# Performance work log

Measured on AMD Instinct MI355X. Metric: run time of the kernel, lower is better.

## Reference

```python
import jax, jax.numpy as jnp
import numpy as np

B, T, N, H = 512, 64, 512, 256  # batch, time steps, input_size, hidden_size
Tm1 = T - 1


def setup_inputs() -> dict:
    key = jax.random.key(0)
    ks = jax.random.split(key, 12)
    s = 0.05
    inp = {
        "input_data": jax.random.normal(ks[0], (B, Tm1, N), dtype=jnp.float32),
        # LSTM params (PyTorch layout: gates ordered i, f, g, o)
        "W_ih": jax.random.normal(ks[1], (4 * H, N), dtype=jnp.float32) * s,
        "W_hh": jax.random.normal(ks[2], (4 * H, H), dtype=jnp.float32) * s,
        "b_ih": jax.random.normal(ks[3], (4 * H,), dtype=jnp.float32) * s,
        "b_hh": jax.random.normal(ks[4], (4 * H,), dtype=jnp.float32) * s,
        # linear_concat: 2H -> T-1
        "Wc": jax.random.normal(ks[5], (Tm1, 2 * H), dtype=jnp.float32) * s,
        "bc": jax.random.normal(ks[6], (Tm1,), dtype=jnp.float32) * s,
        # linear_data: T-1 -> T-1
        "Wd": jax.random.normal(ks[7], (Tm1, Tm1), dtype=jnp.float32) * s,
        "bd": jax.random.normal(ks[8], (Tm1,), dtype=jnp.float32) * s,
        # linear_attn_output: T-1 -> 1
        "Wa": jax.random.normal(ks[9], (1, Tm1), dtype=jnp.float32) * s,
        "ba": jax.random.normal(ks[10], (1,), dtype=jnp.float32) * s,
    }
    return inp


def reference(input_data, W_ih, W_hh, b_ih, b_hh, Wc, bc, Wd, bd, Wa, ba):
    b, tm1, n = input_data.shape
    h_dim = W_hh.shape[1]
    f32 = input_data.dtype

    # linear_data(input_data.permute(0,2,1)) is loop-invariant: [B, N, T-1]
    t2 = jnp.einsum("btn,st->bns", input_data, Wd) + bd

    def step(carry, x_t):  # x_t: [B, N] = input_data[:, t, :]
        h, c = carry  # [B, H] each
        # linear_concat(cat(hidden, state)); repeat over N is a broadcast
        hs = jnp.concatenate([h, c], axis=1)           # [B, 2H]
        t1 = hs @ Wc.T + bc                             # [B, T-1]
        z = jnp.tanh(t1[:, None, :] + t2)               # [B, N, T-1]
        scores = jnp.einsum("bns,s->bn", z, Wa[0]) + ba[0]  # [B, N]
        attn = jax.nn.softmax(scores, axis=1)           # [B, N]
        wx = attn * x_t                                 # [B, N]
        # one-step LSTM cell (PyTorch gate order i, f, g, o)
        gates = wx @ W_ih.T + b_ih + h @ W_hh.T + b_hh  # [B, 4H]
        i, f, g, o = jnp.split(gates, 4, axis=1)
        i = jax.nn.sigmoid(i)
        f = jax.nn.sigmoid(f)
        g = jnp.tanh(g)
        o = jax.nn.sigmoid(o)
        c_new = f * c + i * g
        h_new = o * jnp.tanh(c_new)
        return (h_new, c_new), (wx, h_new, attn)

    h0 = jnp.zeros((b, h_dim), dtype=f32)
    c0 = jnp.zeros((b, h_dim), dtype=f32)
    x_seq = jnp.transpose(input_data, (1, 0, 2))  # [T-1, B, N]
    _, (iw, ie, w) = jax.lax.scan(step, (h0, c0), x_seq)
    input_weighted = jnp.transpose(iw, (1, 0, 2))  # [B, T-1, N]
    input_encoded = jnp.transpose(ie, (1, 0, 2))   # [B, T-1, H]
    weight = jnp.transpose(w, (1, 0, 2))           # [B, T-1, N]
    return input_weighted, input_encoded, weight
```

## Files before the change

### kernel.cpp

```cpp
#include <hip/hip_runtime.h>

typedef unsigned int u32;
typedef _Float16 h1;
typedef _Float16 h2 __attribute__((ext_vector_type(2)));


#define OFF_IE (512*63*512)
#define OFF_W  (512*63*512 + 512*63*256)

#define C2 2.885390081777927f


__device__ __forceinline__ float tanh_fast(float x){
    float e = __builtin_amdgcn_exp2f(x * C2);
    return 1.0f - 2.0f * __builtin_amdgcn_rcpf(e + 1.0f);
}
__device__ __forceinline__ float sigmoid_fast(float x){
    float e = __builtin_amdgcn_exp2f(x * -1.4426950408889634f);
    return __builtin_amdgcn_rcpf(1.0f + e);
}
__device__ __forceinline__ float exp_fast(float x){
    return __builtin_amdgcn_exp2f(x * 1.4426950408889634f);
}
__device__ __forceinline__ float dot2h(u32 a, u32 w, float c){
    return __builtin_amdgcn_fdot2(__builtin_bit_cast(h2, a),
                                  __builtin_bit_cast(h2, w), c, false);
}

__global__ __launch_bounds__(256)
void prep_pack(const float* __restrict__ Wih, const float* __restrict__ Whh,
               const float* __restrict__ bih, const float* __restrict__ bhh,
               const float* __restrict__ Wc,
               u32* __restrict__ WihP, u32* __restrict__ WhhP,
               h1* __restrict__ WcH, float* __restrict__ biasg)
{
    int i = blockIdx.x*256 + threadIdx.x;
    if (i < 262144){
        int k = i >> 8, n2 = i & 255;
        float2 w = *(const float2*)(Wih + (size_t)k*512 + 2*n2);
        h2 p; p[0] = (h1)w.x; p[1] = (h1)w.y;
        WihP[n2*1024 + k] = __builtin_bit_cast(u32, p);
    } else if (i < 393216){
        int j = i - 262144;
        int k = j >> 7, j2 = j & 127;
        float2 w = *(const float2*)(Whh + (size_t)k*256 + 2*j2);
        h2 p; p[0] = (h1)w.x; p[1] = (h1)w.y;
        WhhP[j2*1024 + k] = __builtin_bit_cast(u32, p);
    } else if (i < 425472){
        int j = i - 393216;
        WcH[j] = (h1)(C2 * Wc[j]);
    } else if (i < 426496){
        int k = i - 425472;
        biasg[k] = bih[k] + bhh[k];
    }
}

__global__ __launch_bounds__(256)
void prep_t2(const float* __restrict__ inp, const float* __restrict__ Wd,
             const float* __restrict__ bd, h1* __restrict__ t2)
{
    __shared__ float wd_s[63*63];
    __shared__ float bd_s[63];
    int tid = threadIdx.x;
    for (int i = tid; i < 3969; i += 256) wd_s[i] = Wd[i];
    if (tid < 63) bd_s[tid] = bd[tid];
    __syncthreads();
    int bb = blockIdx.x;
    int n  = blockIdx.y*256 + tid;
    float x[63];
    const float* ip = inp + (size_t)bb*63*512 + n;
    #pragma unroll
    for (int t = 0; t < 63; ++t) x[t] = ip[(size_t)t*512];
    h1* op = t2 + (size_t)bb*63*512 + n;
    for (int s = 0; s < 63; ++s){
        float acc = bd_s[s];
        const float* w = wd_s + s*63;
        #pragma unroll
        for (int t = 0; t < 63; ++t) acc = fmaf(x[t], w[t], acc);
        op[(size_t)s*512] = (h1)(C2 * acc);
    }
}

#define DOTQ(X0, X1, W) \
    a00 = dot2h((X0), (W).x, a00); a01 = dot2h((X0), (W).y, a01); \
    a10 = dot2h((X1), (W).x, a10); a11 = dot2h((X1), (W).y, a11);

#define CONSUME8(BUF, XS0, XS1, J0) { \
    uint4 _p0 = *(const uint4*)&(XS0)[(J0)]; \
    uint4 _p1 = *(const uint4*)&(XS0)[(J0)+4]; \
    uint4 _q0 = *(const uint4*)&(XS1)[(J0)]; \
    uint4 _q1 = *(const uint4*)&(XS1)[(J0)+4]; \
    DOTQ(_p0.x, _q0.x, BUF[0]) DOTQ(_p0.y, _q0.y, BUF[1]) \
    DOTQ(_p0.z, _q0.z, BUF[2]) DOTQ(_p0.w, _q0.w, BUF[3]) \
    DOTQ(_p1.x, _q1.x, BUF[4]) DOTQ(_p1.y, _q1.y, BUF[5]) \
    DOTQ(_p1.z, _q1.z, BUF[6]) DOTQ(_p1.w, _q1.w, BUF[7]) }

#define PRE8(BUF, PTR) { \
    _Pragma("unroll") \
    for (int _u = 0; _u < 8; ++_u) BUF[_u] = (PTR)[_u*512]; \
    (PTR) += 8*512; }

__global__ __launch_bounds__(512, 1)
void encoder_main(const float* __restrict__ inp, const float* __restrict__ bc,
                  const float* __restrict__ Wa, const float* __restrict__ ba,
                  const h1* __restrict__ t2g, const u32* __restrict__ WihP,
                  const u32* __restrict__ WhhP, const h1* __restrict__ WcH,
                  const float* __restrict__ biasg, float* __restrict__ out)
{
    __shared__ u32   t2l[2][256][66];
    __shared__ u32   hcp[2][256];
    __shared__ u32   wxp[2][256];
    __shared__ float t1s[2][64];
    __shared__ float t1p[126][4];
    __shared__ float gates[2][1024];
    __shared__ float red[8];
    __shared__ float wamL[64];

    const int tid = threadIdx.x;
    const int wg  = blockIdx.x;
    const int n2  = tid & 255;
    const int b   = tid >> 8;
    const int bG  = wg*2 + b;

    if (tid < 512){
        hcp[tid >> 8][tid & 255] = 0u;
    }
    if (tid < 64) wamL[tid] = (tid < 63) ? (-2.0f * Wa[tid]) : 0.0f;
    if (tid < 128) ((float*)t1s)[tid] = 0.0f;
    float2 bv = *(const float2*)&biasg[2*tid];
    float bcv = 0.0f;
    if (tid < 126){
        int pb = (tid >= 63) ? 1 : 0;
        bcv = C2 * bc[tid - 63*pb];
    }
    {
        const u32* tg = (const u32*)(t2g + (size_t)bG*63*512);
        u32* trw = &t2l[b][n2][0];
        for (int s = 0; s < 63; ++s) trw[s] = tg[s*256 + n2];
        trw[63] = 0u; trw[64] = 0u; trw[65] = 0u;
    }
    float c_reg = 0.0f;
    __syncthreads();

    for (int t = 0; t < 63; ++t){
        if (tid < 504){
            int oi = tid >> 2, sl = tid & 3;
            int pb = (oi >= 63) ? 1 : 0;
            int s  = oi - 63*pb;
            const uint4* xv4 = (const uint4*)&hcp[pb][sl*64];
            const uint4* wv4 = (const uint4*)(WcH + s*512 + sl*128);
            float acc = 0.f;
            #pragma unroll
            for (int i = 0; i < 16; ++i){
                uint4 x = xv4[i], w = wv4[i];
                acc = dot2h(x.x, w.x, acc);
                acc = dot2h(x.y, w.y, acc);
                acc = dot2h(x.z, w.z, acc);
                acc = dot2h(x.w, w.w, acc);
            }
            t1p[oi][sl] = acc;
        }
        __syncthreads();
        if (tid < 126){
            int pb = (tid >= 63) ? 1 : 0;
            int s  = tid - 63*pb;
            float4 v = *(const float4*)&t1p[tid][0];
            t1s[pb][s] = bcv + v.x + v.y + v.z + v.w;
        }
        __syncthreads();

        float2 xv = *(const float2*)(inp + ((size_t)bG*63 + t)*512 + 2*n2);
        const u32* trow = &t2l[b][n2][0];
        float acc0 = 0.f, acc1 = 0.f;
        #pragma unroll 4
        for (int q = 0; q < 32; ++q){
            uint2 tv = *(const uint2*)(trow + 2*q);
            float2 t1v = *(const float2*)&t1s[b][2*q];
            float2 wv  = *(const float2*)&wamL[2*q];
            h2 va = __builtin_bit_cast(h2, tv.x);
            h2 vb = __builtin_bit_cast(h2, tv.y);
            float r0 = __builtin_amdgcn_rcpf(1.f + __builtin_amdgcn_exp2f(t1v.x + (float)va[0]));
            float r1 = __builtin_amdgcn_rcpf(1.f + __builtin_amdgcn_exp2f(t1v.x + (float)va[1]));
            float r2 = __builtin_amdgcn_rcpf(1.f + __builtin_amdgcn_exp2f(t1v.y + (float)vb[0]));
            float r3 = __builtin_amdgcn_rcpf(1.f + __builtin_amdgcn_exp2f(t1v.y + (float)vb[1]));
            acc0 = fmaf(wv.x, r0, acc0);
            acc1 = fmaf(wv.x, r1, acc1);
            acc0 = fmaf(wv.y, r2, acc0);
            acc1 = fmaf(wv.y, r3, acc1);
        }
        float e0 = exp_fast(acc0);
        float e1 = exp_fast(acc1);
        float es = e0 + e1;
        #pragma unroll
        for (int off = 32; off > 0; off >>= 1) es += __shfl_xor(es, off, 64);
        if ((tid & 63) == 0) red[tid >> 6] = es;
        __syncthreads();
        float tot  = red[b*4+0] + red[b*4+1] + red[b*4+2] + red[b*4+3];
        float rinv = __builtin_amdgcn_rcpf(tot);
        float at0 = e0*rinv, at1 = e1*rinv;
        float wx0 = at0*xv.x, wx1 = at1*xv.y;
        {
            float2* po = (float2*)(out + ((size_t)bG*63 + t)*512) + n2;
            *po = make_float2(wx0, wx1);
            float2* pa = (float2*)(out + OFF_W + ((size_t)bG*63 + t)*512) + n2;
            *pa = make_float2(at0, at1);
            h2 p; p[0] = (h1)wx0; p[1] = (h1)wx1;
            wxp[b][n2] = __builtin_bit_cast(u32, p);
        }
        __syncthreads();

        float a00 = 0.f, a01 = 0.f, a10 = 0.f, a11 = 0.f;
        {
            const uint2* wp = (const uint2*)WihP + tid;
            uint2 W0[8], W1[8];
            PRE8(W0, wp)
            PRE8(W1, wp)
            #pragma unroll 1
            for (int jb = 0; jb < 16; ++jb){
                CONSUME8(W0, wxp[0], wxp[1], jb*16)
                PRE8(W0, wp)
                CONSUME8(W1, wxp[0], wxp[1], jb*16 + 8)
                PRE8(W1, wp)
            }
        }
        {
            const uint2* wq = (const uint2*)WhhP + tid;
            uint2 W0[8], W1[8];
            PRE8(W0, wq)
            PRE8(W1, wq)
            #pragma unroll 1
            for (int jb = 0; jb < 8; ++jb){
                CONSUME8(W0, hcp[0], hcp[1], jb*16)
                PRE8(W0, wq)
                CONSUME8(W1, hcp[0], hcp[1], jb*16 + 8)
                PRE8(W1, wq)
            }
        }
        *(float2*)&gates[0][2*tid] = make_float2(a00 + bv.x, a01 + bv.y);
        *(float2*)&gates[1][2*tid] = make_float2(a10 + bv.x, a11 + bv.y);
        __syncthreads();

        {
            int j = n2;
            float gi = gates[b][j],     gf = gates[b][j+256];
            float gg = gates[b][j+512], go = gates[b][j+768];
            float iv = sigmoid_fast(gi), fv = sigmoid_fast(gf);
            float gv = tanh_fast(gg),    ov = sigmoid_fast(go);
            float cn = fmaf(fv, c_reg, iv*gv);
            c_reg = cn;
            float hn = ov * tanh_fast(cn);
            ((h1*)&hcp[b][0])[j]   = (h1)hn;
            ((h1*)&hcp[b][128])[j] = (h1)cn;
            out[OFF_IE + ((size_t)bG*63 + t)*256 + j] = hn;
        }
        __syncthreads();
    }
}

extern "C" void kernel_launch(void* const* d_in, const int* in_sizes, int n_in,
                              void* d_out, int out_size, void* d_ws, size_t ws_size,
                              hipStream_t stream)
{
    const float* inp = (const float*)d_in[0];
    const float* Wih = (const float*)d_in[1];
    const float* Whh = (const float*)d_in[2];
    const float* bih = (const float*)d_in[3];
    const float* bhh = (const float*)d_in[4];
    const float* Wc  = (const float*)d_in[5];
    const float* bc  = (const float*)d_in[6];
    const float* Wd  = (const float*)d_in[7];
    const float* bd  = (const float*)d_in[8];
    const float* Wa  = (const float*)d_in[9];
    const float* ba  = (const float*)d_in[10];
    float* out = (float*)d_out;

    char* ws = (char*)d_ws;
    h1*    t2    = (h1*)ws;
    u32*   WihP  = (u32*)(ws + 33030144);
    u32*   WhhP  = (u32*)(ws + 34078720);
    h1*    WcH   = (h1*)(ws + 34603008);
    float* biasg = (float*)(ws + 34667520);

    prep_pack<<<1666, 256, 0, stream>>>(Wih, Whh, bih, bhh, Wc, WihP, WhhP, WcH, biasg);
    prep_t2<<<dim3(512, 2), 256, 0, stream>>>(inp, Wd, bd, t2);
    encoder_main<<<256, 512, 0, stream>>>(inp, bc, Wa, ba, t2, WihP, WhhP, WcH, biasg, out);
}
```

Before: 2.126 ms.

## Overlap W_hh gate matvec with attention tanh loop, stagger weight reads per block

The recurrent W_hh·h matvec is moved to run interleaved with the attention-score exp/rcp loop, since both depend only on the previous hidden state. This lets global weight loads and dot products overlap the transcendental work. Weight prefetch grows from 8- to 16-deep buffers, and each workgroup starts its weight sweep at a different offset (slot = wg>>3) to spread L2 traffic across blocks. __syncthreads is replaced with a barrier that waits only on LDS counters, so outstanding global loads and stores do not stall the barrier. The deeper buffers raise register pressure, and the custom barrier depends on the compiler honouring the memory clobbers.

New measurement: 2.439 ms. +14.7%, slower.

```diff
diff --git a/kernel.cpp b/kernel.cpp
--- a/kernel.cpp
+++ b/kernel.cpp
@@ -25,6 +25,12 @@
 __device__ __forceinline__ float dot2h(u32 a, u32 w, float c){
     return __builtin_amdgcn_fdot2(__builtin_bit_cast(h2, a),
                                   __builtin_bit_cast(h2, w), c, false);
+}
+
+__device__ __forceinline__ void bar_lgkm(){
+    asm volatile("s_waitcnt lgkmcnt(0)" ::: "memory");
+    __builtin_amdgcn_s_barrier();
+    asm volatile("" ::: "memory");
 }
 
 __global__ __launch_bounds__(256)
@@ -85,20 +91,33 @@
     a00 = dot2h((X0), (W).x, a00); a01 = dot2h((X0), (W).y, a01); \
     a10 = dot2h((X1), (W).x, a10); a11 = dot2h((X1), (W).y, a11);
 
-#define CONSUME8(BUF, XS0, XS1, J0) { \
-    uint4 _p0 = *(const uint4*)&(XS0)[(J0)]; \
-    uint4 _p1 = *(const uint4*)&(XS0)[(J0)+4]; \
-    uint4 _q0 = *(const uint4*)&(XS1)[(J0)]; \
-    uint4 _q1 = *(const uint4*)&(XS1)[(J0)+4]; \
-    DOTQ(_p0.x, _q0.x, BUF[0]) DOTQ(_p0.y, _q0.y, BUF[1]) \
-    DOTQ(_p0.z, _q0.z, BUF[2]) DOTQ(_p0.w, _q0.w, BUF[3]) \
-    DOTQ(_p1.x, _q1.x, BUF[4]) DOTQ(_p1.y, _q1.y, BUF[5]) \
-    DOTQ(_p1.z, _q1.z, BUF[6]) DOTQ(_p1.w, _q1.w, BUF[7]) }
-
-#define PRE8(BUF, PTR) { \
-    _Pragma("unroll") \
-    for (int _u = 0; _u < 8; ++_u) BUF[_u] = (PTR)[_u*512]; \
-    (PTR) += 8*512; }
+#define PRE16(BUF, PTR) { const uint2* _pp = (PTR); \
+    _Pragma("unroll") for (int _u = 0; _u < 16; ++_u) BUF[_u] = _pp[_u*512]; }
+
+#define CONSUME16(BUF, XS0, XS1, J0) { \
+    uint4 _p0 = *(const uint4*)&(XS0)[(J0)];     uint4 _q0 = *(const uint4*)&(XS1)[(J0)]; \
+    uint4 _p1 = *(const uint4*)&(XS0)[(J0)+4];   uint4 _q1 = *(const uint4*)&(XS1)[(J0)+4]; \
+    uint4 _p2 = *(const uint4*)&(XS0)[(J0)+8];   uint4 _q2 = *(const uint4*)&(XS1)[(J0)+8]; \
+    uint4 _p3 = *(const uint4*)&(XS0)[(J0)+12];  uint4 _q3 = *(const uint4*)&(XS1)[(J0)+12]; \
+    DOTQ(_p0.x,_q0.x,BUF[0])  DOTQ(_p0.y,_q0.y,BUF[1])  DOTQ(_p0.z,_q0.z,BUF[2])  DOTQ(_p0.w,_q0.w,BUF[3]) \
+    DOTQ(_p1.x,_q1.x,BUF[4])  DOTQ(_p1.y,_q1.y,BUF[5])  DOTQ(_p1.z,_q1.z,BUF[6])  DOTQ(_p1.w,_q1.w,BUF[7]) \
+    DOTQ(_p2.x,_q2.x,BUF[8])  DOTQ(_p2.y,_q2.y,BUF[9])  DOTQ(_p2.z,_q2.z,BUF[10]) DOTQ(_p2.w,_q2.w,BUF[11]) \
+    DOTQ(_p3.x,_q3.x,BUF[12]) DOTQ(_p3.y,_q3.y,BUF[13]) DOTQ(_p3.z,_q3.z,BUF[14]) DOTQ(_p3.w,_q3.w,BUF[15]) }
+
+#define P2_ITER(Q) { \
+    uint2 tv = *(const uint2*)(trow + 2*(Q)); \
+    float2 t1v = *(const float2*)&t1s[b][2*(Q)]; \
+    float2 wv  = *(const float2*)&wamL[2*(Q)]; \
+    h2 va = __builtin_bit_cast(h2, tv.x); \
+    h2 vb = __builtin_bit_cast(h2, tv.y); \
+    float r0 = __builtin_amdgcn_rcpf(1.f + __builtin_amdgcn_exp2f(t1v.x + (float)va[0])); \
+    float r1 = __builtin_amdgcn_rcpf(1.f + __builtin_amdgcn_exp2f(t1v.x + (float)va[1])); \
+    float r2 = __builtin_amdgcn_rcpf(1.f + __builtin_amdgcn_exp2f(t1v.y + (float)vb[0])); \
+    float r3 = __builtin_amdgcn_rcpf(1.f + __builtin_amdgcn_exp2f(t1v.y + (float)vb[1])); \
+    acc0 = fmaf(wv.x, r0, acc0); \
+    acc1 = fmaf(wv.x, r1, acc1); \
+    acc0 = fmaf(wv.y, r2, acc0); \
+    acc1 = fmaf(wv.y, r3, acc1); }
 
 __global__ __launch_bounds__(512, 1)
 void encoder_main(const float* __restrict__ inp, const float* __restrict__ bc,
@@ -122,6 +141,11 @@
     const int b   = tid >> 8;
     const int bG  = wg*2 + b;
 
+    const int slot = wg >> 3;
+    const int s_ih = slot & 15;
+    const int s_hh = slot & 7;
+    const int sp1  = slot & 15;
+
     if (tid < 512){
         hcp[tid >> 8][tid & 255] = 0u;
     }
@@ -140,9 +164,14 @@
         trw[63] = 0u; trw[64] = 0u; trw[65] = 0u;
     }
     float c_reg = 0.0f;
+    const uint2* ibase = (const uint2*)WihP + tid;
+    const uint2* hbase = (const uint2*)WhhP + tid;
     __syncthreads();
 
     for (int t = 0; t < 63; ++t){
+        float2 xv = *(const float2*)(inp + ((size_t)bG*63 + t)*512 + 2*n2);
+        uint2 H0[16], H1[16];
+        PRE16(H0, hbase + s_hh*8192)
         if (tid < 504){
             int oi = tid >> 2, sl = tid & 3;
             int pb = (oi >= 63) ? 1 : 0;
@@ -151,7 +180,8 @@
             const uint4* wv4 = (const uint4*)(WcH + s*512 + sl*128);
             float acc = 0.f;
             #pragma unroll
-            for (int i = 0; i < 16; ++i){
+            for (int ii = 0; ii < 16; ++ii){
+                int i = ii + sp1; if (i >= 16) i -= 16;
                 uint4 x = xv4[i], w = wv4[i];
                 acc = dot2h(x.x, w.x, acc);
                 acc = dot2h(x.y, w.y, acc);
@@ -160,33 +190,39 @@
             }
             t1p[oi][sl] = acc;
         }
-        __syncthreads();
+        bar_lgkm();
         if (tid < 126){
             int pb = (tid >= 63) ? 1 : 0;
             int s  = tid - 63*pb;
             float4 v = *(const float4*)&t1p[tid][0];
             t1s[pb][s] = bcv + v.x + v.y + v.z + v.w;
         }
-        __syncthreads();
-
-        float2 xv = *(const float2*)(inp + ((size_t)bG*63 + t)*512 + 2*n2);
+        bar_lgkm();
+
+        float acc0 = 0.f, acc1 = 0.f;
+        float a00 = 0.f, a01 = 0.f, a10 = 0.f, a11 = 0.f;
         const u32* trow = &t2l[b][n2][0];
-        float acc0 = 0.f, acc1 = 0.f;
-        #pragma unroll 4
-        for (int q = 0; q < 32; ++q){
-            uint2 tv = *(const uint2*)(trow + 2*q);
-            float2 t1v = *(const float2*)&t1s[b][2*q];
-            float2 wv  = *(const float2*)&wamL[2*q];
-            h2 va = __builtin_bit_cast(h2, tv.x);
-            h2 vb = __builtin_bit_cast(h2, tv.y);
-            float r0 = __builtin_amdgcn_rcpf(1.f + __builtin_amdgcn_exp2f(t1v.x + (float)va[0]));
-            float r1 = __builtin_amdgcn_rcpf(1.f + __builtin_amdgcn_exp2f(t1v.x + (float)va[1]));
-            float r2 = __builtin_amdgcn_rcpf(1.f + __builtin_amdgcn_exp2f(t1v.y + (float)vb[0]));
-            float r3 = __builtin_amdgcn_rcpf(1.f + __builtin_amdgcn_exp2f(t1v.y + (float)vb[1]));
-            acc0 = fmaf(wv.x, r0, acc0);
-            acc1 = fmaf(wv.x, r1, acc1);
-            acc0 = fmaf(wv.y, r2, acc0);
-            acc1 = fmaf(wv.y, r3, acc1);
+        int hb = s_hh;
+        #pragma unroll 1
+        for (int i2 = 0; i2 < 3; ++i2){
+            int hb1 = hb + 1;  if (hb1 >= 8) hb1 -= 8;
+            int hb2 = hb1 + 1; if (hb2 >= 8) hb2 -= 8;
+            int q0 = 8*i2;
+            P2_ITER(q0+0) P2_ITER(q0+1) P2_ITER(q0+2) P2_ITER(q0+3)
+            PRE16(H1, hbase + hb1*8192)
+            CONSUME16(H0, hcp[0], hcp[1], hb*16)
+            P2_ITER(q0+4) P2_ITER(q0+5) P2_ITER(q0+6) P2_ITER(q0+7)
+            PRE16(H0, hbase + hb2*8192)
+            CONSUME16(H1, hcp[0], hcp[1], hb1*16)
+            hb = hb2;
+        }
+        {
+            int hb1 = hb + 1; if (hb1 >= 8) hb1 -= 8;
+            P2_ITER(24) P2_ITER(25) P2_ITER(26) P2_ITER(27)
+            PRE16(H1, hbase + hb1*8192)
+            CONSUME16(H0, hcp[0], hcp[1], hb*16)
+            P2_ITER(28) P2_ITER(29) P2_ITER(30) P2_ITER(31)
+            CONSUME16(H1, hcp[0], hcp[1], hb1*16)
         }
         float e0 = exp_fast(acc0);
         float e1 = exp_fast(acc1);
@@ -194,11 +230,12 @@
         #pragma unroll
         for (int off = 32; off > 0; off >>= 1) es += __shfl_xor(es, off, 64);
         if ((tid & 63) == 0) red[tid >> 6] = es;
-        __syncthreads();
+        bar_lgkm();
         float tot  = red[b*4+0] + red[b*4+1] + red[b*4+2] + red[b*4+3];
         float rinv = __builtin_amdgcn_rcpf(tot);
         float at0 = e0*rinv, at1 = e1*rinv;
         float wx0 = at0*xv.x, wx1 = at1*xv.y;
+        uint2 W0[16], W1[16];
         {
             float2* po = (float2*)(out + ((size_t)bG*63 + t)*512) + n2;
             *po = make_float2(wx0, wx1);
@@ -207,38 +244,29 @@
             h2 p; p[0] = (h1)wx0; p[1] = (h1)wx1;
             wxp[b][n2] = __builtin_bit_cast(u32, p);
         }
-        __syncthreads();
-
-        float a00 = 0.f, a01 = 0.f, a10 = 0.f, a11 = 0.f;
+        int ib = s_ih;
+        PRE16(W0, ibase + ib*8192)
+        bar_lgkm();
+
+        #pragma unroll 1
+        for (int i2 = 0; i2 < 7; ++i2){
+            int ib1 = ib + 1;  if (ib1 >= 16) ib1 -= 16;
+            int ib2 = ib1 + 1; if (ib2 >= 16) ib2 -= 16;
+            PRE16(W1, ibase + ib1*8192)
+            CONSUME16(W0, wxp[0], wxp[1], ib*16)
+            PRE16(W0, ibase + ib2*8192)
+            CONSUME16(W1, wxp[0], wxp[1], ib1*16)
+            ib = ib2;
+        }
         {
-            const uint2* wp = (const uint2*)WihP + tid;
-            uint2 W0[8], W1[8];
-            PRE8(W0, wp)
-            PRE8(W1, wp)
-            #pragma unroll 1
-            for (int jb = 0; jb < 16; ++jb){
-                CONSUME8(W0, wxp[0], wxp[1], jb*16)
-                PRE8(W0, wp)
-                CONSUME8(W1, wxp[0], wxp[1], jb*16 + 8)
-                PRE8(W1, wp)
-            }
-        }
-        {
-            const uint2* wq = (const uint2*)WhhP + tid;
-            uint2 W0[8], W1[8];
-            PRE8(W0, wq)
-            PRE8(W1, wq)
-            #pragma unroll 1
-            for (int jb = 0; jb < 8; ++jb){
-                CONSUME8(W0, hcp[0], hcp[1], jb*16)
-                PRE8(W0, wq)
-                CONSUME8(W1, hcp[0], hcp[1], jb*16 + 8)
-                PRE8(W1, wq)
-            }
+            int ib1 = ib + 1; if (ib1 >= 16) ib1 -= 16;
+            PRE16(W1, ibase + ib1*8192)
+            CONSUME16(W0, wxp[0], wxp[1], ib*16)
+            CONSUME16(W1, wxp[0], wxp[1], ib1*16)
         }
         *(float2*)&gates[0][2*tid] = make_float2(a00 + bv.x, a01 + bv.y);
         *(float2*)&gates[1][2*tid] = make_float2(a10 + bv.x, a11 + bv.y);
-        __syncthreads();
+        bar_lgkm();
 
         {
             int j = n2;
@@ -253,7 +281,7 @@
             ((h1*)&hcp[b][128])[j] = (h1)cn;
             out[OFF_IE + ((size_t)bG*63 + t)*256 + j] = hn;
         }
-        __syncthreads();
+        bar_lgkm();
     }
 }
 
```
